# Kernel optimization log

Measured on AMD Instinct MI355X. Metric: run time of the kernel, lower is better.

The kernel has to match this reference:

```python
import jax, jax.numpy as jnp
import numpy as np

B, TE, TD, D = 8, 2048, 2048, 256

def setup_inputs() -> dict:
    key = jax.random.key(0)
    k1, k2 = jax.random.split(key)
    encoder_outputs = jax.random.normal(k1, (B, TE, D), dtype=jnp.float32)
    decoder_outputs = jax.random.normal(k2, (B, TD, D), dtype=jnp.float32)
    return {"encoder_outputs": encoder_outputs, "decoder_outputs": decoder_outputs}

def reference(encoder_outputs, decoder_outputs):
    # luong_score[b,e,t] = sum_d enc[b,e,d] * dec[b,t,d]   (batch_dot with dec transposed)
    luong_score = jnp.einsum('bed,btd->bet', encoder_outputs, decoder_outputs)
    # softmax over encoder-time axis (axis=1)
    luong_score = jax.nn.softmax(luong_score, axis=1)
    # original does expand_dims + broadcast-multiply + sum over axis=1;
    # same math as a contraction over e: context[b,t,d] = sum_e score[b,e,t]*enc[b,e,d]
    encoder_vector = jnp.einsum('bet,bed->btd', luong_score, encoder_outputs)
    return jnp.concatenate([decoder_outputs, encoder_vector], axis=-1)
```

## Files before the change

### kernel.cpp

```cpp
#include <hip/hip_runtime.h>

typedef _Float16 f16;
typedef _Float16 f16x4 __attribute__((ext_vector_type(4)));
typedef _Float16 f16x8 __attribute__((ext_vector_type(8)));
typedef float    f32x4 __attribute__((ext_vector_type(4)));

#define NB   8
#define TE   2048
#define TD   2048
#define DIM  256
#define NSPLIT 3
#define LOG2E 1.44269504088896340736f

#define AS1(p) ((const __attribute__((address_space(1))) void*)(p))
#define AS3(p) ((__attribute__((address_space(3))) void*)(p))
#define MFMA16(a,b,c) __builtin_amdgcn_mfma_f32_16x16x32_f16((a),(b),(c),0,0,0)

__device__ __forceinline__ unsigned lds_u32(void* p) {
    return (unsigned)(size_t)((__attribute__((address_space(3))) void*)p);
}
__device__ __forceinline__ f16x4 tr_rd0(unsigned a) {
    f16x4 r;
    asm volatile("ds_read_b64_tr_b16 %0, %1" : "=v"(r) : "v"(a));
    return r;
}
__device__ __forceinline__ f16x4 tr_rd1(unsigned a) {
    f16x4 r;
    asm volatile("ds_read_b64_tr_b16 %0, %1 offset:2048" : "=v"(r) : "v"(a));
    return r;
}

__global__ __launch_bounds__(256) void prep_kernel(const float* __restrict__ enc,
                                                   f16* __restrict__ ench) {
    size_t i = ((size_t)blockIdx.x * 256 + threadIdx.x) * 8;
    float4 v0 = *(const float4*)(enc + i);
    float4 v1 = *(const float4*)(enc + i + 4);
    f16x8 o;
    o[0]=(f16)v0.x; o[1]=(f16)v0.y; o[2]=(f16)v0.z; o[3]=(f16)v0.w;
    o[4]=(f16)v1.x; o[5]=(f16)v1.y; o[6]=(f16)v1.z; o[7]=(f16)v1.w;
    *(f16x8*)(ench + i) = o;
}

#define LDS_P  32768
#define LDS_X  37888

__global__ __launch_bounds__(256, 3) void attn_kernel(
        const float* __restrict__ dec32,
        const f16*  __restrict__ enc_h,
        f16*   __restrict__ ctxp,
        float* __restrict__ m_arr,
        float* __restrict__ l_arr,
        int nsplit) {
    __shared__ __align__(16) char lds[38400];
    const int tid  = threadIdx.x;
    const int lane = tid & 63;
    const int wv   = tid >> 6;
    const int th   = wv >> 1;
    const int eh   = wv & 1;
    const int tcol = lane & 15;
    const int q    = lane >> 4;

    int fid = blockIdx.x + 32 * (blockIdx.y + 8 * blockIdx.z);
    const int b  = fid & 7;
    const int xb = (fid >> 3) & 31;
    const int z  = fid >> 8;
    const int t0 = xb * 64;
    const int tile0 = (64 * z) / nsplit;
    const int tile1 = (64 * (z + 1)) / nsplit;
    const int iters = tile1 - tile0;

    const char* encb = (const char*)(enc_h + (size_t)b * TE * DIM);

    const int c0  = wv * 64 + lane;
    const int e_l = ((c0 >> 7) << 2) | ((c0 >> 1) & 3);
    const int d_l = (((c0 >> 3) & 15) << 4) | ((c0 & 1) << 3);
    const int stage_goff = e_l * (DIM * 2) + d_l * 2;
    char* stage_dst = lds + wv * 1024;

    const int qk_base = (eh * 4 + (tcol >> 2)) * 2048 + (q >> 1) * 128 + (tcol & 3) * 32 + (q & 1) * 16;
    const unsigned pv_base = (unsigned)(q * 4096 + eh * 1024 + tcol * 8);
    const unsigned lds_base = lds_u32(lds);
    char* pb = lds + LDS_P + th * 2560;
    float* exch = (float*)(lds + LDS_X);

    f16x8 qf[2][8];
    {
        const float* qp = dec32 + ((size_t)b * TD + t0 + th * 32) * DIM;
        #pragma unroll
        for (int tn = 0; tn < 2; tn++)
            #pragma unroll
            for (int ks = 0; ks < 8; ks++) {
                const float* p = qp + (size_t)(tn * 16 + tcol) * DIM + ks * 32 + q * 8;
                float4 u = *(const float4*)(p);
                float4 v = *(const float4*)(p + 4);
                f16x8 o;
                o[0]=(f16)u.x; o[1]=(f16)u.y; o[2]=(f16)u.z; o[3]=(f16)u.w;
                o[4]=(f16)v.x; o[5]=(f16)v.y; o[6]=(f16)v.z; o[7]=(f16)v.w;
                qf[tn][ks] = o;
            }
    }

    {
        const char* s = encb + (size_t)tile0 * 16384 + stage_goff;
        #pragma unroll
        for (int i = 0; i < 4; i++)
            __builtin_amdgcn_global_load_lds(AS1(s + i * 4096), AS3(stage_dst + i * 4096), 16, 0, 0);
    }

    const f32x4 zero4 = {0.f, 0.f, 0.f, 0.f};
    float m_[2] = {-INFINITY, -INFINITY};
    float l_[2] = {0.f, 0.f};
    f32x4 ctx[8][2];
    #pragma unroll
    for (int dm = 0; dm < 8; dm++) { ctx[dm][0] = zero4; ctx[dm][1] = zero4; }

    __syncthreads();

    for (int it = 0; it < iters; ++it) {
        const int nat = (it & 1) << 14;
        f32x4 st[2] = {zero4, zero4};
        const char* natp = lds + nat + qk_base;
        #pragma unroll
        for (int ks = 0; ks < 8; ks++) {
            f16x8 af = *(const f16x8*)(natp + ks * 256);
            st[0] = MFMA16(af, qf[0][ks], st[0]);
            st[1] = MFMA16(af, qf[1][ks], st[1]);
        }
        float mx[2];
        #pragma unroll
        for (int tn = 0; tn < 2; tn++) {
            float m0 = fmaxf(fmaxf(st[tn][0], st[tn][1]), fmaxf(st[tn][2], st[tn][3]));
            m0 = fmaxf(m0, __shfl_xor(m0, 16, 64));
            m0 = fmaxf(m0, __shfl_xor(m0, 32, 64));
            mx[tn] = m0;
        }
        if (q == 0) { exch[wv * 32 + tcol] = mx[0]; exch[wv * 32 + 16 + tcol] = mx[1]; }
        __syncthreads();
        if (it + 1 < iters) {
            const char* s = encb + (size_t)(tile0 + it + 1) * 16384 + stage_goff;
            char* dd = stage_dst + (((it + 1) & 1) << 14);
            #pragma unroll
            for (int i = 0; i < 4; i++)
                __builtin_amdgcn_global_load_lds(AS1(s + i * 4096), AS3(dd + i * 4096), 16, 0, 0);
        }
        bool anyb = false;
        float al[2], s4v[2];
        #pragma unroll
        for (int tn = 0; tn < 2; tn++) {
            float ox = exch[(wv ^ 1) * 32 + tn * 16 + tcol];
            float mn = fmaxf(m_[tn], fmaxf(mx[tn], ox));
            al[tn] = __builtin_amdgcn_exp2f((m_[tn] - mn) * LOG2E);
            anyb = anyb || (mn > m_[tn]);
            m_[tn] = mn;
            f16x4 pv;
            #pragma unroll
            for (int r = 0; r < 4; r++)
                pv[r] = (f16)__builtin_amdgcn_exp2f((st[tn][r] - mn) * LOG2E);
            *(f16x4*)(pb + (tn * 16 + tcol) * 80 + eh * 32 + q * 8) = pv;
            float s4 = ((float)pv[0] + (float)pv[1]) + ((float)pv[2] + (float)pv[3]);
            s4 += __shfl_xor(s4, 16, 64);
            s4 += __shfl_xor(s4, 32, 64);
            s4v[tn] = s4;
        }
        if (__any(anyb)) {
            #pragma unroll
            for (int tn = 0; tn < 2; tn++) {
                l_[tn] *= al[tn];
                #pragma unroll
                for (int dm = 0; dm < 8; dm++) {
                    ctx[dm][tn][0] *= al[tn]; ctx[dm][tn][1] *= al[tn];
                    ctx[dm][tn][2] *= al[tn]; ctx[dm][tn][3] *= al[tn];
                }
            }
        }
        l_[0] += s4v[0]; l_[1] += s4v[1];
        __syncthreads();
        f16x8 pf0 = *(const f16x8*)(pb + tcol * 80 + q * 16);
        f16x8 pf1 = *(const f16x8*)(pb + (16 + tcol) * 80 + q * 16);
        const unsigned trb = lds_base + (unsigned)nat + pv_base;
        f16x4 tr[16];
        #pragma unroll
        for (int dm = 0; dm < 8; dm++) {
            tr[2 * dm]     = tr_rd0(trb + (unsigned)(dm * 128));
            tr[2 * dm + 1] = tr_rd1(trb + (unsigned)(dm * 128));
        }
        asm volatile("s_waitcnt lgkmcnt(0)" ::: "memory");
        __builtin_amdgcn_sched_barrier(0);
        #pragma unroll
        for (int dm = 0; dm < 8; dm++) {
            f16x8 af = __builtin_shufflevector(tr[2 * dm], tr[2 * dm + 1], 0, 1, 2, 3, 4, 5, 6, 7);
            ctx[dm][0] = MFMA16(af, pf0, ctx[dm][0]);
            ctx[dm][1] = MFMA16(af, pf1, ctx[dm][1]);
        }
    }

    if (q == 0) { exch[wv * 32 + tcol] = l_[0]; exch[wv * 32 + 16 + tcol] = l_[1]; }
    __syncthreads();
    float lt[2];
    lt[0] = l_[0] + exch[(wv ^ 1) * 32 + tcol];
    lt[1] = l_[1] + exch[(wv ^ 1) * 32 + 16 + tcol];
    size_t row0 = (size_t)(z * NB + b) * TD + t0 + th * 32;
    #pragma unroll
    for (int tn = 0; tn < 2; tn++) {
        float inv = 1.0f / lt[tn];
        size_t rb = (row0 + tn * 16 + tcol) * DIM + eh * 128;
        #pragma unroll
        for (int dm = 0; dm < 8; dm++) {
            f16x4 cv;
            #pragma unroll
            for (int r = 0; r < 4; r++) cv[r] = (f16)(ctx[dm][tn][r] * inv);
            *(f16x4*)(ctxp + rb + dm * 16 + q * 4) = cv;
        }
    }
    if (eh == 0 && q == 0) {
        int mi = (z * NB + b) * TD + t0 + th * 32 + tcol;
        m_arr[mi]      = m_[0];
        m_arr[mi + 16] = m_[1];
        l_arr[mi]      = lt[0];
        l_arr[mi + 16] = lt[1];
    }
}

__global__ __launch_bounds__(256) void combine_kernel(const float* __restrict__ dec32,
        const f16* __restrict__ ctxp, const float* __restrict__ m_arr,
        const float* __restrict__ l_arr, float* __restrict__ out, int nsplit) {
    int idx  = blockIdx.x * 256 + threadIdx.x;
    int trow = idx >> 5;
    int dg   = (idx & 31) * 8;
    float m0[NSPLIT], l0[NSPLIT], M = -INFINITY;
    #pragma unroll
    for (int s = 0; s < NSPLIT; s++) if (s < nsplit) {
        m0[s] = m_arr[s * (NB * TD) + trow];
        l0[s] = l_arr[s * (NB * TD) + trow];
        M = fmaxf(M, m0[s]);
    }
    float L = 0.f, w[NSPLIT];
    #pragma unroll
    for (int s = 0; s < NSPLIT; s++) if (s < nsplit) {
        w[s] = __builtin_amdgcn_exp2f((m0[s] - M) * LOG2E) * l0[s];
        L += w[s];
    }
    float invL = 1.0f / L;
    float acc[8] = {0.f,0.f,0.f,0.f,0.f,0.f,0.f,0.f};
    #pragma unroll
    for (int s = 0; s < NSPLIT; s++) if (s < nsplit) {
        f16x8 v = *(const f16x8*)(ctxp + ((size_t)s * (NB * TD) + trow) * DIM + dg);
        float ws = w[s] * invL;
        #pragma unroll
        for (int j = 0; j < 8; j++) acc[j] += ws * (float)v[j];
    }
    float4 d0 = *(const float4*)(dec32 + (size_t)trow * DIM + dg);
    float4 d1 = *(const float4*)(dec32 + (size_t)trow * DIM + dg + 4);
    float* ob = out + (size_t)trow * 512;
    *(float4*)(ob + dg)     = d0;
    *(float4*)(ob + dg + 4) = d1;
    float4 c0, c1;
    c0.x=acc[0]; c0.y=acc[1]; c0.z=acc[2]; c0.w=acc[3];
    c1.x=acc[4]; c1.y=acc[5]; c1.z=acc[6]; c1.w=acc[7];
    *(float4*)(ob + 256 + dg)     = c0;
    *(float4*)(ob + 256 + dg + 4) = c1;
}

extern "C" void kernel_launch(void* const* d_in, const int* in_sizes, int n_in,
                              void* d_out, int out_size, void* d_ws, size_t ws_size,
                              hipStream_t stream) {
    (void)in_sizes; (void)n_in;
    const float* enc = (const float*)d_in[0];
    const float* dec = (const float*)d_in[1];
    float* out = (float*)d_out;

    const size_t MLB = (size_t)NSPLIT * NB * TD * 4;
    const size_t HB  = (size_t)NB * TE * DIM * 2;
    const size_t CSL = (size_t)NB * TD * DIM * 2;

    float* m_arr = (float*)d_ws;
    float* l_arr = (float*)((char*)d_ws + MLB);
    f16*   ench  = (f16*)((char*)d_ws + 2 * MLB);
    f16*   ctxp  = (f16*)((char*)d_ws + 2 * MLB + HB);

    int nsplit;
    if      (ws_size >= 2 * MLB + HB + 3 * CSL) nsplit = 3;
    else if (ws_size >= 2 * MLB + HB + 2 * CSL) nsplit = 2;
    else { hipMemsetAsync(d_out, 0, (size_t)out_size * sizeof(float), stream); return; }

    prep_kernel<<<2048, 256, 0, stream>>>(enc, ench);
    attn_kernel<<<dim3(32, 8, nsplit), 256, 0, stream>>>(dec, ench, ctxp, m_arr, l_arr, nsplit);
    combine_kernel<<<2048, 256, 0, stream>>>(dec, ctxp, m_arr, l_arr, out, nsplit);
}
```

Before: 170.0 us.

## Switch attention to 32x32 MFMA tiles with per-wave rows and four-way encoder split

Each wave now owns 32 decoder rows and uses 32x32x16 MFMA for both the score and context products, which removes the cross-wave max/sum exchange and one block barrier per iteration. The encoder dimension is split four ways with a fixed 16 tiles each, occupancy drops to 2 blocks per CU, and the last split writes fp32 context straight into the output buffer. Max and sum are packed as fp16 pairs, with the running max rounded to fp16, which reduces workspace traffic in the combine step but adds rounding risk. Register pressure rises from the 16-wide accumulators.

```diff
diff --git a/kernel.cpp b/kernel.cpp
--- a/kernel.cpp
+++ b/kernel.cpp
@@ -1,20 +1,22 @@
 #include <hip/hip_runtime.h>
 
 typedef _Float16 f16;
+typedef _Float16 f16x2 __attribute__((ext_vector_type(2)));
 typedef _Float16 f16x4 __attribute__((ext_vector_type(4)));
 typedef _Float16 f16x8 __attribute__((ext_vector_type(8)));
-typedef float    f32x4 __attribute__((ext_vector_type(4)));
+typedef float    f32x16 __attribute__((ext_vector_type(16)));
 
 #define NB   8
 #define TE   2048
 #define TD   2048
 #define DIM  256
-#define NSPLIT 3
+#define NBTD (NB * TD)
 #define LOG2E 1.44269504088896340736f
 
 #define AS1(p) ((const __attribute__((address_space(1))) void*)(p))
 #define AS3(p) ((__attribute__((address_space(3))) void*)(p))
-#define MFMA16(a,b,c) __builtin_amdgcn_mfma_f32_16x16x32_f16((a),(b),(c),0,0,0)
+#define MFMA32(a,b,c) __builtin_amdgcn_mfma_f32_32x32x16_f16((a),(b),(c),0,0,0)
+#define SHUF8(x,y) __builtin_shufflevector((x),(y),0,1,2,3,4,5,6,7)
 
 __device__ __forceinline__ unsigned lds_u32(void* p) {
     return (unsigned)(size_t)((__attribute__((address_space(3))) void*)p);
@@ -41,33 +43,27 @@
     *(f16x8*)(ench + i) = o;
 }
 
-#define LDS_P  32768
-#define LDS_X  37888
-
-__global__ __launch_bounds__(256, 3) void attn_kernel(
+__global__ __launch_bounds__(256, 2) void attn_kernel(
         const float* __restrict__ dec32,
         const f16*  __restrict__ enc_h,
         f16*   __restrict__ ctxp,
-        float* __restrict__ m_arr,
-        float* __restrict__ l_arr,
-        int nsplit) {
-    __shared__ __align__(16) char lds[38400];
+        f16x2* __restrict__ ml,
+        float* __restrict__ out) {
+    __shared__ __align__(16) char lds[43008];
     const int tid  = threadIdx.x;
     const int lane = tid & 63;
     const int wv   = tid >> 6;
-    const int th   = wv >> 1;
-    const int eh   = wv & 1;
-    const int tcol = lane & 15;
-    const int q    = lane >> 4;
-
-    int fid = blockIdx.x + 32 * (blockIdx.y + 8 * blockIdx.z);
-    const int b  = fid & 7;
-    const int xb = (fid >> 3) & 31;
-    const int z  = fid >> 8;
-    const int t0 = xb * 64;
-    const int tile0 = (64 * z) / nsplit;
-    const int tile1 = (64 * (z + 1)) / nsplit;
-    const int iters = tile1 - tile0;
+    const int t5   = lane & 31;
+    const int hi   = lane >> 5;
+
+    const int fid = blockIdx.x + 16 * (blockIdx.y + 8 * blockIdx.z);
+    const int b    = fid & 7;
+    const int rest = fid >> 3;
+    const int xb   = rest & 15;
+    const int z    = rest >> 4;
+    const int t0   = xb * 128 + wv * 32;
+    const int tile0 = z * 16;
+    const int ITERS = 16;
 
     const char* encb = (const char*)(enc_h + (size_t)b * TE * DIM);
 
@@ -77,27 +73,23 @@
     const int stage_goff = e_l * (DIM * 2) + d_l * 2;
     char* stage_dst = lds + wv * 1024;
 
-    const int qk_base = (eh * 4 + (tcol >> 2)) * 2048 + (q >> 1) * 128 + (tcol & 3) * 32 + (q & 1) * 16;
-    const unsigned pv_base = (unsigned)(q * 4096 + eh * 1024 + tcol * 8);
+    const int qk_base = ((lane & 31) >> 2) * 2048 + (lane & 3) * 32 + hi * 16;
+    const unsigned tr_base = (unsigned)(hi * 4096 + ((lane >> 4) & 1) * 128 + (lane & 15) * 8);
     const unsigned lds_base = lds_u32(lds);
-    char* pb = lds + LDS_P + th * 2560;
-    float* exch = (float*)(lds + LDS_X);
-
-    f16x8 qf[2][8];
+    char* pb = lds + 32768 + wv * 2560;
+
+    f16x8 qf[16];
     {
-        const float* qp = dec32 + ((size_t)b * TD + t0 + th * 32) * DIM;
-        #pragma unroll
-        for (int tn = 0; tn < 2; tn++)
-            #pragma unroll
-            for (int ks = 0; ks < 8; ks++) {
-                const float* p = qp + (size_t)(tn * 16 + tcol) * DIM + ks * 32 + q * 8;
-                float4 u = *(const float4*)(p);
-                float4 v = *(const float4*)(p + 4);
-                f16x8 o;
-                o[0]=(f16)u.x; o[1]=(f16)u.y; o[2]=(f16)u.z; o[3]=(f16)u.w;
-                o[4]=(f16)v.x; o[5]=(f16)v.y; o[6]=(f16)v.z; o[7]=(f16)v.w;
-                qf[tn][ks] = o;
-            }
+        const float* qrow = dec32 + ((size_t)b * TD + t0 + t5) * DIM + hi * 8;
+        #pragma unroll
+        for (int ks = 0; ks < 16; ks++) {
+            float4 u = *(const float4*)(qrow + ks * 16);
+            float4 v = *(const float4*)(qrow + ks * 16 + 4);
+            f16x8 o;
+            o[0]=(f16)u.x; o[1]=(f16)u.y; o[2]=(f16)u.z; o[3]=(f16)u.w;
+            o[4]=(f16)v.x; o[5]=(f16)v.y; o[6]=(f16)v.z; o[7]=(f16)v.w;
+            qf[ks] = o;
+        }
     }
 
     {
@@ -107,147 +99,160 @@
             __builtin_amdgcn_global_load_lds(AS1(s + i * 4096), AS3(stage_dst + i * 4096), 16, 0, 0);
     }
 
-    const f32x4 zero4 = {0.f, 0.f, 0.f, 0.f};
-    float m_[2] = {-INFINITY, -INFINITY};
-    float l_[2] = {0.f, 0.f};
-    f32x4 ctx[8][2];
-    #pragma unroll
-    for (int dm = 0; dm < 8; dm++) { ctx[dm][0] = zero4; ctx[dm][1] = zero4; }
+    float m_ = -INFINITY, l_ = 0.f;
+    f32x16 ctx[8];
+    #pragma unroll
+    for (int dm = 0; dm < 8; dm++)
+        #pragma unroll
+        for (int r = 0; r < 16; r++) ctx[dm][r] = 0.f;
 
     __syncthreads();
 
-    for (int it = 0; it < iters; ++it) {
+    for (int it = 0; it < ITERS; ++it) {
         const int nat = (it & 1) << 14;
-        f32x4 st[2] = {zero4, zero4};
-        const char* natp = lds + nat + qk_base;
-        #pragma unroll
-        for (int ks = 0; ks < 8; ks++) {
-            f16x8 af = *(const f16x8*)(natp + ks * 256);
-            st[0] = MFMA16(af, qf[0][ks], st[0]);
-            st[1] = MFMA16(af, qf[1][ks], st[1]);
-        }
-        float mx[2];
-        #pragma unroll
-        for (int tn = 0; tn < 2; tn++) {
-            float m0 = fmaxf(fmaxf(st[tn][0], st[tn][1]), fmaxf(st[tn][2], st[tn][3]));
-            m0 = fmaxf(m0, __shfl_xor(m0, 16, 64));
-            m0 = fmaxf(m0, __shfl_xor(m0, 32, 64));
-            mx[tn] = m0;
-        }
-        if (q == 0) { exch[wv * 32 + tcol] = mx[0]; exch[wv * 32 + 16 + tcol] = mx[1]; }
-        __syncthreads();
-        if (it + 1 < iters) {
+        if (it + 1 < ITERS) {
             const char* s = encb + (size_t)(tile0 + it + 1) * 16384 + stage_goff;
-            char* dd = stage_dst + (((it + 1) & 1) << 14);
+            char* dd = lds + (((it + 1) & 1) << 14) + wv * 1024;
             #pragma unroll
             for (int i = 0; i < 4; i++)
                 __builtin_amdgcn_global_load_lds(AS1(s + i * 4096), AS3(dd + i * 4096), 16, 0, 0);
         }
-        bool anyb = false;
-        float al[2], s4v[2];
-        #pragma unroll
-        for (int tn = 0; tn < 2; tn++) {
-            float ox = exch[(wv ^ 1) * 32 + tn * 16 + tcol];
-            float mn = fmaxf(m_[tn], fmaxf(mx[tn], ox));
-            al[tn] = __builtin_amdgcn_exp2f((m_[tn] - mn) * LOG2E);
-            anyb = anyb || (mn > m_[tn]);
-            m_[tn] = mn;
+        f32x16 st;
+        #pragma unroll
+        for (int r = 0; r < 16; r++) st[r] = 0.f;
+        const char* natp = lds + nat + qk_base;
+        #pragma unroll
+        for (int ks = 0; ks < 16; ks++) {
+            f16x8 af = *(const f16x8*)(natp + ks * 128);
+            st = MFMA32(af, qf[ks], st);
+        }
+        float x0 = fmaxf(fmaxf(st[0], st[1]),  fmaxf(st[2], st[3]));
+        float x1 = fmaxf(fmaxf(st[4], st[5]),  fmaxf(st[6], st[7]));
+        float x2 = fmaxf(fmaxf(st[8], st[9]),  fmaxf(st[10], st[11]));
+        float x3 = fmaxf(fmaxf(st[12], st[13]), fmaxf(st[14], st[15]));
+        float mx = fmaxf(fmaxf(x0, x1), fmaxf(x2, x3));
+        mx = fmaxf(mx, __shfl_xor(mx, 32, 64));
+        float ms = (float)(f16)fmaxf(m_, mx);
+        float al = __builtin_amdgcn_exp2f((m_ - ms) * LOG2E);
+        bool bump = ms > m_;
+        m_ = ms;
+        float ssum = 0.f;
+        #pragma unroll
+        for (int g = 0; g < 4; g++) {
             f16x4 pv;
             #pragma unroll
-            for (int r = 0; r < 4; r++)
-                pv[r] = (f16)__builtin_amdgcn_exp2f((st[tn][r] - mn) * LOG2E);
-            *(f16x4*)(pb + (tn * 16 + tcol) * 80 + eh * 32 + q * 8) = pv;
-            float s4 = ((float)pv[0] + (float)pv[1]) + ((float)pv[2] + (float)pv[3]);
-            s4 += __shfl_xor(s4, 16, 64);
-            s4 += __shfl_xor(s4, 32, 64);
-            s4v[tn] = s4;
-        }
-        if (__any(anyb)) {
-            #pragma unroll
-            for (int tn = 0; tn < 2; tn++) {
-                l_[tn] *= al[tn];
+            for (int r = 0; r < 4; r++) {
+                float p = __builtin_amdgcn_exp2f((st[4 * g + r] - ms) * LOG2E);
+                pv[r] = (f16)p;
+                ssum += (float)pv[r];
+            }
+            *(f16x4*)(pb + t5 * 80 + g * 16 + hi * 8) = pv;
+        }
+        ssum += __shfl_xor(ssum, 32, 64);
+        l_ = l_ * al + ssum;
+        if (__any(bump)) {
+            #pragma unroll
+            for (int dm = 0; dm < 8; dm++)
                 #pragma unroll
-                for (int dm = 0; dm < 8; dm++) {
-                    ctx[dm][tn][0] *= al[tn]; ctx[dm][tn][1] *= al[tn];
-                    ctx[dm][tn][2] *= al[tn]; ctx[dm][tn][3] *= al[tn];
-                }
+                for (int r = 0; r < 16; r++) ctx[dm][r] *= al;
+        }
+        const unsigned trb = lds_base + (unsigned)nat + tr_base;
+        #pragma unroll
+        for (int ks = 0; ks < 2; ks++) {
+            f16x8 pf = *(const f16x8*)(pb + t5 * 80 + ks * 32 + hi * 16);
+            const unsigned ab = trb + (unsigned)(ks * 8192);
+            f16x4 a0 = tr_rd0(ab);        f16x4 a1 = tr_rd1(ab);
+            f16x4 a2 = tr_rd0(ab + 256);  f16x4 a3 = tr_rd1(ab + 256);
+            f16x4 a4 = tr_rd0(ab + 512);  f16x4 a5 = tr_rd1(ab + 512);
+            f16x4 a6 = tr_rd0(ab + 768);  f16x4 a7 = tr_rd1(ab + 768);
+            asm volatile("s_waitcnt lgkmcnt(0)" ::: "memory");
+            __builtin_amdgcn_sched_barrier(0);
+            ctx[0] = MFMA32(SHUF8(a0, a1), pf, ctx[0]);
+            ctx[1] = MFMA32(SHUF8(a2, a3), pf, ctx[1]);
+            ctx[2] = MFMA32(SHUF8(a4, a5), pf, ctx[2]);
+            ctx[3] = MFMA32(SHUF8(a6, a7), pf, ctx[3]);
+            f16x4 b0 = tr_rd0(ab + 1024); f16x4 b1 = tr_rd1(ab + 1024);
+            f16x4 b2 = tr_rd0(ab + 1280); f16x4 b3 = tr_rd1(ab + 1280);
+            f16x4 b4 = tr_rd0(ab + 1536); f16x4 b5 = tr_rd1(ab + 1536);
+            f16x4 b6 = tr_rd0(ab + 1792); f16x4 b7 = tr_rd1(ab + 1792);
+            asm volatile("s_waitcnt lgkmcnt(0)" ::: "memory");
+            __builtin_amdgcn_sched_barrier(0);
+            ctx[4] = MFMA32(SHUF8(b0, b1), pf, ctx[4]);
+            ctx[5] = MFMA32(SHUF8(b2, b3), pf, ctx[5]);
+            ctx[6] = MFMA32(SHUF8(b4, b5), pf, ctx[6]);
+            ctx[7] = MFMA32(SHUF8(b6, b7), pf, ctx[7]);
+        }
+        __syncthreads();
+    }
+
+    const float inv = 1.0f / l_;
+    if (z < 3) {
+        f16* cb = ctxp + ((size_t)(z * NB + b) * TD + t0 + t5) * DIM;
+        #pragma unroll
+        for (int dm = 0; dm < 8; dm++)
+            #pragma unroll
+            for (int g = 0; g < 4; g++) {
+                f16x4 cv;
+                #pragma unroll
+                for (int r = 0; r < 4; r++) cv[r] = (f16)(ctx[dm][4 * g + r] * inv);
+                *(f16x4*)(cb + dm * 32 + g * 8 + hi * 4) = cv;
             }
-        }
-        l_[0] += s4v[0]; l_[1] += s4v[1];
-        __syncthreads();
-        f16x8 pf0 = *(const f16x8*)(pb + tcol * 80 + q * 16);
-        f16x8 pf1 = *(const f16x8*)(pb + (16 + tcol) * 80 + q * 16);
-        const unsigned trb = lds_base + (unsigned)nat + pv_base;
-        f16x4 tr[16];
-        #pragma unroll
-        for (int dm = 0; dm < 8; dm++) {
-            tr[2 * dm]     = tr_rd0(trb + (unsigned)(dm * 128));
-            tr[2 * dm + 1] = tr_rd1(trb + (unsigned)(dm * 128));
-        }
-        asm volatile("s_waitcnt lgkmcnt(0)" ::: "memory");
-        __builtin_amdgcn_sched_barrier(0);
-        #pragma unroll
-        for (int dm = 0; dm < 8; dm++) {
-            f16x8 af = __builtin_shufflevector(tr[2 * dm], tr[2 * dm + 1], 0, 1, 2, 3, 4, 5, 6, 7);
-            ctx[dm][0] = MFMA16(af, pf0, ctx[dm][0]);
-            ctx[dm][1] = MFMA16(af, pf1, ctx[dm][1]);
-        }
-    }
-
-    if (q == 0) { exch[wv * 32 + tcol] = l_[0]; exch[wv * 32 + 16 + tcol] = l_[1]; }
-    __syncthreads();
-    float lt[2];
-    lt[0] = l_[0] + exch[(wv ^ 1) * 32 + tcol];
-    lt[1] = l_[1] + exch[(wv ^ 1) * 32 + 16 + tcol];
-    size_t row0 = (size_t)(z * NB + b) * TD + t0 + th * 32;
-    #pragma unroll
-    for (int tn = 0; tn < 2; tn++) {
-        float inv = 1.0f / lt[tn];
-        size_t rb = (row0 + tn * 16 + tcol) * DIM + eh * 128;
-        #pragma unroll
-        for (int dm = 0; dm < 8; dm++) {
-            f16x4 cv;
-            #pragma unroll
-            for (int r = 0; r < 4; r++) cv[r] = (f16)(ctx[dm][tn][r] * inv);
-            *(f16x4*)(ctxp + rb + dm * 16 + q * 4) = cv;
-        }
-    }
-    if (eh == 0 && q == 0) {
-        int mi = (z * NB + b) * TD + t0 + th * 32 + tcol;
-        m_arr[mi]      = m_[0];
-        m_arr[mi + 16] = m_[1];
-        l_arr[mi]      = lt[0];
-        l_arr[mi + 16] = lt[1];
+    } else {
+        float* ob = out + ((size_t)b * TD + t0 + t5) * 512 + 256;
+        #pragma unroll
+        for (int dm = 0; dm < 8; dm++)
+            #pragma unroll
+            for (int g = 0; g < 4; g++) {
+                float4 cv;
+                cv.x = ctx[dm][4 * g]     * inv;
+                cv.y = ctx[dm][4 * g + 1] * inv;
+                cv.z = ctx[dm][4 * g + 2] * inv;
+                cv.w = ctx[dm][4 * g + 3] * inv;
+                *(float4*)(ob + dm * 32 + g * 8 + hi * 4) = cv;
+            }
+    }
+    if (hi == 0) {
+        f16x2 v; v[0] = (f16)m_; v[1] = (f16)l_;
+        ml[(size_t)z * NBTD + (size_t)b * TD + t0 + t5] = v;
     }
 }
 
 __global__ __launch_bounds__(256) void combine_kernel(const float* __restrict__ dec32,
-        const f16* __restrict__ ctxp, const float* __restrict__ m_arr,
-        const float* __restrict__ l_arr, float* __restrict__ out, int nsplit) {
+        const f16* __restrict__ ctxp, const f16x2* __restrict__ ml,
+        float* __restrict__ out) {
     int idx  = blockIdx.x * 256 + threadIdx.x;
     int trow = idx >> 5;
     int dg   = (idx & 31) * 8;
-    float m0[NSPLIT], l0[NSPLIT], M = -INFINITY;
-    #pragma unroll
-    for (int s = 0; s < NSPLIT; s++) if (s < nsplit) {
-        m0[s] = m_arr[s * (NB * TD) + trow];
-        l0[s] = l_arr[s * (NB * TD) + trow];
+    float m0[4], l0[4], M = -INFINITY;
+    #pragma unroll
+    for (int s = 0; s < 4; s++) {
+        f16x2 v = ml[(size_t)s * NBTD + trow];
+        m0[s] = (float)v[0];
+        l0[s] = (float)v[1];
         M = fmaxf(M, m0[s]);
     }
-    float L = 0.f, w[NSPLIT];
-    #pragma unroll
-    for (int s = 0; s < NSPLIT; s++) if (s < nsplit) {
+    float L = 0.f, w[4];
+    #pragma unroll
+    for (int s = 0; s < 4; s++) {
         w[s] = __builtin_amdgcn_exp2f((m0[s] - M) * LOG2E) * l0[s];
         L += w[s];
     }
     float invL = 1.0f / L;
     float acc[8] = {0.f,0.f,0.f,0.f,0.f,0.f,0.f,0.f};
     #pragma unroll
-    for (int s = 0; s < NSPLIT; s++) if (s < nsplit) {
-        f16x8 v = *(const f16x8*)(ctxp + ((size_t)s * (NB * TD) + trow) * DIM + dg);
+    for (int s = 0; s < 3; s++) {
+        f16x8 v = *(const f16x8*)(ctxp + ((size_t)s * NBTD + trow) * DIM + dg);
         float ws = w[s] * invL;
         #pragma unroll
         for (int j = 0; j < 8; j++) acc[j] += ws * (float)v[j];
+    }
+    {
+        const float* o3 = out + (size_t)trow * 512 + 256 + dg;
+        float4 p0 = *(const float4*)(o3);
+        float4 p1 = *(const float4*)(o3 + 4);
+        float w3 = w[3] * invL;
+        acc[0] += w3 * p0.x; acc[1] += w3 * p0.y; acc[2] += w3 * p0.z; acc[3] += w3 * p0.w;
+        acc[4] += w3 * p1.x; acc[5] += w3 * p1.y; acc[6] += w3 * p1.z; acc[7] += w3 * p1.w;
     }
     float4 d0 = *(const float4*)(dec32 + (size_t)trow * DIM + dg);
     float4 d1 = *(const float4*)(dec32 + (size_t)trow * DIM + dg + 4);
@@ -269,21 +274,20 @@
     const float* dec = (const float*)d_in[1];
     float* out = (float*)d_out;
 
-    const size_t MLB = (size_t)NSPLIT * NB * TD * 4;
+    const size_t MLB = (size_t)4 * NBTD * 4;
     const size_t HB  = (size_t)NB * TE * DIM * 2;
-    const size_t CSL = (size_t)NB * TD * DIM * 2;
-
-    float* m_arr = (float*)d_ws;
-    float* l_arr = (float*)((char*)d_ws + MLB);
-    f16*   ench  = (f16*)((char*)d_ws + 2 * MLB);
-    f16*   ctxp  = (f16*)((char*)d_ws + 2 * MLB + HB);
-
-    int nsplit;
-    if      (ws_size >= 2 * MLB + HB + 3 * CSL) nsplit = 3;
-    else if (ws_size >= 2 * MLB + HB + 2 * CSL) nsplit = 2;
-    else { hipMemsetAsync(d_out, 0, (size_t)out_size * sizeof(float), stream); return; }
+    const size_t CSL = (size_t)NBTD * DIM * 2;
+    const size_t NEED = MLB + HB + 3 * CSL;
+
+    if (ws_size < NEED) {
+        hipMemsetAsync(d_out, 0, (size_t)out_size * sizeof(float), stream);
+        return;
+    }
+    f16x2* ml   = (f16x2*)d_ws;
+    f16*   ench = (f16*)((char*)d_ws + MLB);
+    f16*   ctxp = (f16*)((char*)d_ws + MLB + HB);
 
     prep_kernel<<<2048, 256, 0, stream>>>(enc, ench);
-    attn_kernel<<<dim3(32, 8, nsplit), 256, 0, stream>>>(dec, ench, ctxp, m_arr, l_arr, nsplit);
-    combine_kernel<<<2048, 256, 0, stream>>>(dec, ctxp, m_arr, l_arr, out, nsplit);
-}
+    attn_kernel<<<dim3(16, 8, 4), 256, 0, stream>>>(dec, ench, ctxp, ml, out);
+    combine_kernel<<<2048, 256, 0, stream>>>(dec, ctxp, ml, out);
+}
```

Measured after the change: 145.6 us. 1.17x faster.
